# Optimization experiments

Hardware: AMD Instinct MI355X
Metric: run time of the kernel (lower is better)

## Reference

```python
import jax, jax.numpy as jnp
import numpy as np

EPS_LN = 1e-5
NEG_SLOPE = 0.2
NUM_GRAPHS = 64


def layer_norm(h, g, b):
    mu = h.mean(-1, keepdims=True)
    var = ((h - mu) ** 2).mean(-1, keepdims=True)
    return (h - mu) * jax.lax.rsqrt(var + EPS_LN) * g + b


def segment_softmax(alpha, dst, n):
    # alpha: [E2, H], softmax over edges sharing the same dst node
    m = jax.ops.segment_max(alpha, dst, num_segments=n)
    m = jnp.where(jnp.isfinite(m), m, 0.0)
    e = jnp.exp(alpha - m[dst])
    s = jax.ops.segment_sum(e, dst, num_segments=n)
    return e / (s[dst] + 1e-16)


def gat_conv(h, src, dst, eattr, W, We, a_s, a_d, a_e, bias, H, C):
    # PyG GATConv: shared src/dst linear, edge features, self-loops (fill='mean')
    N = h.shape[0]
    x = (h @ W).reshape(N, H, C)  # [N,H,C]
    loop = jnp.arange(N)
    src2 = jnp.concatenate([src, loop])
    dst2 = jnp.concatenate([dst, loop])
    loop_attr = jnp.broadcast_to(eattr.mean(0, keepdims=True), (N, eattr.shape[1]))
    e2 = jnp.concatenate([eattr, loop_attr], 0)
    eh = (e2 @ We).reshape(-1, H, C)  # [E2,H,C]
    alpha = (x * a_s).sum(-1)[src2] + (x * a_d).sum(-1)[dst2] + (eh * a_e).sum(-1)
    alpha = jax.nn.leaky_relu(alpha, NEG_SLOPE)  # [E2,H]
    alpha = segment_softmax(alpha, dst2, N)
    out = jax.ops.segment_sum(x[src2] * alpha[:, :, None], dst2, num_segments=N)
    return out.reshape(N, H * C) + bias


def setup_inputs():
    key = jax.random.key(0)
    ks = jax.random.split(key, 24)
    N, E = 50000, 400000
    Fin, Hd, H, ed = 6, 64, 4, 1
    d0 = Hd * H          # 256 after layer0
    C1 = 128 // H        # 32, layer1 per-head out
    s = 0.1
    inp = {
        'x': jax.random.normal(ks[0], (N, Fin), jnp.float32),
        'edge_index': jax.random.randint(ks[1], (2, E), 0, N),
        'edge_attr': jax.random.uniform(ks[2], (E, ed), jnp.float32),
        'batch': jnp.sort(jax.random.randint(ks[3], (N,), 0, NUM_GRAPHS)),
        'W_in': jax.random.normal(ks[4], (Fin, Hd), jnp.float32) * s,
        'b_in': jnp.zeros((Hd,), jnp.float32),
        'l0_W': jax.random.normal(ks[5], (Hd, H * Hd), jnp.float32) * s,
        'l0_We': jax.random.normal(ks[6], (ed, H * Hd), jnp.float32) * s,
        'l0_as': jax.random.normal(ks[7], (H, Hd), jnp.float32) * s,
        'l0_ad': jax.random.normal(ks[8], (H, Hd), jnp.float32) * s,
        'l0_ae': jax.random.normal(ks[9], (H, Hd), jnp.float32) * s,
        'l0_b': jnp.zeros((H * Hd,), jnp.float32),
        'ln0_g': jnp.ones((d0,), jnp.float32),
        'ln0_b': jnp.zeros((d0,), jnp.float32),
        'l1_W': jax.random.normal(ks[10], (d0, H * C1), jnp.float32) * s,
        'l1_We': jax.random.normal(ks[11], (ed, H * C1), jnp.float32) * s,
        'l1_as': jax.random.normal(ks[12], (H, C1), jnp.float32) * s,
        'l1_ad': jax.random.normal(ks[13], (H, C1), jnp.float32) * s,
        'l1_ae': jax.random.normal(ks[14], (H, C1), jnp.float32) * s,
        'l1_b': jnp.zeros((H * C1,), jnp.float32),
        'ln1_g': jnp.ones((128,), jnp.float32),
        'ln1_b': jnp.zeros((128,), jnp.float32),
    }
    return inp


def reference(x, edge_index, edge_attr, batch, W_in, b_in,
              l0_W, l0_We, l0_as, l0_ad, l0_ae, l0_b, ln0_g, ln0_b,
              l1_W, l1_We, l1_as, l1_ad, l1_ae, l1_b, ln1_g, ln1_b):
    src, dst = edge_index[0], edge_index[1]
    H = 4
    h = x @ W_in + b_in                                  # input_proj
    h = gat_conv(h, src, dst, edge_attr, l0_W, l0_We, l0_as, l0_ad, l0_ae, l0_b, H, 64)
    h = layer_norm(h, ln0_g, ln0_b)
    h = jax.nn.elu(h)                                    # dropout off (eval)
    h = gat_conv(h, src, dst, edge_attr, l1_W, l1_We, l1_as, l1_ad, l1_ae, l1_b, H, 32)
    h = layer_norm(h, ln1_g, ln1_b)
    cnt = jax.ops.segment_sum(jnp.ones((h.shape[0],), h.dtype), batch, num_segments=NUM_GRAPHS)
    h_mean = jax.ops.segment_sum(h, batch, num_segments=NUM_GRAPHS) / jnp.maximum(cnt, 1.0)[:, None]
    h_max = jax.ops.segment_max(h, batch, num_segments=NUM_GRAPHS)
    return (h_mean + h_max) / 2.0
```

## Files before the change

kernel.cpp:

```cpp
#include <hip/hip_runtime.h>
#include <math.h>

#define EPS_LN   1e-5f
#define NEG_SLOPE 0.2f
#define NUM_GRAPHS 64
#define POOL_SPLIT 16

__device__ __forceinline__ float red64(float v) {
    #pragma unroll
    for (int m = 32; m > 0; m >>= 1) v += __shfl_xor(v, m);
    return v;
}

__global__ __launch_bounds__(256) void k_input_proj(
    const float* __restrict__ x, const float* __restrict__ Win,
    const float* __restrict__ bin, float* __restrict__ h, int N)
{
    int t = blockIdx.x * 256 + threadIdx.x;
    if (t >= N * 64) return;
    int n = t >> 6, c = t & 63;
    float acc = bin[c];
    const float* xr = x + n * 6;
    #pragma unroll
    for (int k = 0; k < 6; ++k) acc += xr[k] * Win[k * 64 + c];
    h[t] = acc;
}

__global__ __launch_bounds__(256) void k_prep(
    const float* __restrict__ We0, const float* __restrict__ ae0,
    const float* __restrict__ We1, const float* __restrict__ ae1,
    float* __restrict__ wedot0, float* __restrict__ wedot1)
{
    __shared__ float red[256];
    int t = threadIdx.x;
    red[t] = We0[t] * ae0[t];
    __syncthreads();
    for (int s = 32; s > 0; s >>= 1) { if ((t & 63) < s) red[t] += red[t + s]; __syncthreads(); }
    if ((t & 63) == 0) wedot0[t >> 6] = red[t];
    __syncthreads();
    red[t] = (t < 128) ? We1[t] * ae1[t] : 0.f;
    __syncthreads();
    for (int s = 16; s > 0; s >>= 1) { if (t < 128 && (t & 31) < s) red[t] += red[t + s]; __syncthreads(); }
    if (t < 128 && (t & 31) == 0) wedot1[t >> 5] = red[t];
}

__global__ __launch_bounds__(256) void k_esum_partial(const float* __restrict__ ea, float* __restrict__ part, int E)
{
    __shared__ float red[256];
    int t = threadIdx.x;
    float s = 0.f;
    for (int i = blockIdx.x * 256 + t; i < E; i += gridDim.x * 256) s += ea[i];
    red[t] = s; __syncthreads();
    for (int k = 128; k > 0; k >>= 1) { if (t < k) red[t] += red[t + k]; __syncthreads(); }
    if (t == 0) part[blockIdx.x] = red[0];
}
__global__ __launch_bounds__(256) void k_esum_final(const float* __restrict__ part, int B, float* __restrict__ mean_out, int E)
{
    __shared__ float red[256];
    int t = threadIdx.x;
    red[t] = (t < B) ? part[t] : 0.f; __syncthreads();
    for (int k = 128; k > 0; k >>= 1) { if (t < k) red[t] += red[t + k]; __syncthreads(); }
    if (t == 0) *mean_out = red[0] / (float)E;
}

__global__ __launch_bounds__(256) void k_counts_init(int* __restrict__ counts, int N)
{
    int t = blockIdx.x * 256 + threadIdx.x;
    if (t < N) counts[t] = 1;
}
__global__ __launch_bounds__(256) void k_count(const int* __restrict__ dst, int* __restrict__ counts, int E)
{
    int e = blockIdx.x * 256 + threadIdx.x;
    if (e < E) atomicAdd(&counts[dst[e]], 1);
}
__global__ __launch_bounds__(256) void k_scan_partial(const int* __restrict__ counts, int* __restrict__ bsum, int N)
{
    __shared__ int red[256];
    int b = blockIdx.x, t = threadIdx.x;
    int base = b * 1024 + t * 4;
    int s = 0;
    #pragma unroll
    for (int i = 0; i < 4; ++i) { int idx = base + i; if (idx < N) s += counts[idx]; }
    red[t] = s; __syncthreads();
    for (int k = 128; k > 0; k >>= 1) { if (t < k) red[t] += red[t + k]; __syncthreads(); }
    if (t == 0) bsum[b] = red[0];
}
__global__ __launch_bounds__(64) void k_scan_bsums(const int* __restrict__ bsum, int* __restrict__ bpre, int B)
{
    __shared__ int s[64];
    int t = threadIdx.x;
    int v = (t < B) ? bsum[t] : 0;
    s[t] = v; __syncthreads();
    for (int off = 1; off < 64; off <<= 1) {
        int u = (t >= off) ? s[t - off] : 0; __syncthreads();
        s[t] += u; __syncthreads();
    }
    if (t < B) bpre[t] = s[t] - v;
}
__global__ __launch_bounds__(256) void k_scan_chunk(
    const int* __restrict__ counts, const int* __restrict__ bpre,
    int* __restrict__ row_ptr, int* __restrict__ cursor, int N, int E2)
{
    __shared__ int s[256];
    int b = blockIdx.x, t = threadIdx.x;
    int base = b * 1024 + t * 4;
    int l0 = (base + 0 < N) ? counts[base + 0] : 0;
    int l1 = (base + 1 < N) ? counts[base + 1] : 0;
    int l2 = (base + 2 < N) ? counts[base + 2] : 0;
    int l3 = (base + 3 < N) ? counts[base + 3] : 0;
    int lsum = l0 + l1 + l2 + l3;
    s[t] = lsum; __syncthreads();
    for (int off = 1; off < 256; off <<= 1) {
        int u = (t >= off) ? s[t - off] : 0; __syncthreads();
        s[t] += u; __syncthreads();
    }
    int run = bpre[b] + s[t] - lsum;
    if (base + 0 < N) { row_ptr[base + 0] = run; cursor[base + 0] = run; } run += l0;
    if (base + 1 < N) { row_ptr[base + 1] = run; cursor[base + 1] = run; } run += l1;
    if (base + 2 < N) { row_ptr[base + 2] = run; cursor[base + 2] = run; } run += l2;
    if (base + 3 < N) { row_ptr[base + 3] = run; cursor[base + 3] = run; }
    if (b == 0 && t == 0) row_ptr[N] = E2;
}
__global__ __launch_bounds__(256) void k_place(
    const int* __restrict__ dst, int* __restrict__ cursor, int* __restrict__ eids, int E, int N)
{
    int e = blockIdx.x * 256 + threadIdx.x;
    if (e >= E + N) return;
    int d = (e < E) ? dst[e] : (e - E);
    int pos = atomicAdd(&cursor[d], 1);
    eids[pos] = e;
}
__global__ __launch_bounds__(256) void k_rowsort(const int* __restrict__ row_ptr, int* __restrict__ eids, int N)
{
    int n = blockIdx.x * 256 + threadIdx.x;
    if (n >= N) return;
    int r0 = row_ptr[n], r1 = row_ptr[n + 1];
    for (int i = r0 + 1; i < r1; ++i) {
        int key = eids[i];
        int j = i - 1;
        while (j >= r0 && eids[j] > key) { eids[j + 1] = eids[j]; --j; }
        eids[j + 1] = key;
    }
}

#define G0_NPW 4
__global__ __launch_bounds__(256) void k_gemm0(
    const float* __restrict__ h, const float* __restrict__ W0,
    const float* __restrict__ As, const float* __restrict__ Ad,
    float* __restrict__ x0, float* __restrict__ as0, float* __restrict__ ad0, int N)
{
    __shared__ float Wl[64 * 256];
    int t = threadIdx.x;
    for (int i = t; i < 64 * 256; i += 256) Wl[i] = W0[i];
    __syncthreads();
    int wave = t >> 6, lane = t & 63;
    float asv[4], adv[4];
    #pragma unroll
    for (int j = 0; j < 4; ++j) { asv[j] = As[j * 64 + lane]; adv[j] = Ad[j * 64 + lane]; }
    int gw = blockIdx.x * 4 + wave;
    int stride = gridDim.x * 4 * G0_NPW;
    for (int nb = gw * G0_NPW; nb < N; nb += stride) {
        float hv[G0_NPW];
        float acc[G0_NPW][4] = {};
        #pragma unroll
        for (int p = 0; p < G0_NPW; ++p) {
            int n = nb + p;
            hv[p] = (n < N) ? h[(size_t)n * 64 + lane] : 0.f;
        }
        for (int k = 0; k < 64; ++k) {
            float w0 = Wl[k * 256 + lane];
            float w1 = Wl[k * 256 + lane + 64];
            float w2 = Wl[k * 256 + lane + 128];
            float w3 = Wl[k * 256 + lane + 192];
            #pragma unroll
            for (int p = 0; p < G0_NPW; ++p) {
                float hk = __shfl(hv[p], k);
                acc[p][0] += hk * w0; acc[p][1] += hk * w1;
                acc[p][2] += hk * w2; acc[p][3] += hk * w3;
            }
        }
        #pragma unroll
        for (int p = 0; p < G0_NPW; ++p) {
            int n = nb + p;
            if (n < N) {
                float* o = x0 + (size_t)n * 256;
                o[lane] = acc[p][0]; o[lane + 64] = acc[p][1];
                o[lane + 128] = acc[p][2]; o[lane + 192] = acc[p][3];
            }
            #pragma unroll
            for (int j = 0; j < 4; ++j) {
                float ps = red64(acc[p][j] * asv[j]);
                float pd = red64(acc[p][j] * adv[j]);
                if (lane == 0 && n < N) { as0[n * 4 + j] = ps; ad0[n * 4 + j] = pd; }
            }
        }
    }
}

__global__ __launch_bounds__(256) void k_gemm1(
    const float* __restrict__ h0, const float* __restrict__ W1,
    const float* __restrict__ As, const float* __restrict__ Ad,
    float* __restrict__ x1, float* __restrict__ as1, float* __restrict__ ad1, int N)
{
    __shared__ float Wc[32 * 128];
    __shared__ float Ht[32 * 128];
    const int nb = blockIdx.x * 128;
    const int t = threadIdx.x;
    const int tc = t & 15, tr = t >> 4;
    const int r0 = tr * 4, c0 = tc * 4;
    const int kg = t & 7, rb = t >> 3;
    float asv[8], adv[8];
    #pragma unroll
    for (int j = 0; j < 8; ++j) {
        int col = c0 + ((j < 4) ? j : 60 + j);
        asv[j] = As[col]; adv[j] = Ad[col];
    }
    float acc[8][8] = {};
    for (int kc = 0; kc < 8; ++kc) {
        __syncthreads();
        #pragma unroll
        for (int j = 0; j < 4; ++j) {
            int row = rb + j * 32;
            int n = nb + row;
            float4 v = make_float4(0.f, 0.f, 0.f, 0.f);
            if (n < N)
                v = *reinterpret_cast<const float4*>(h0 + (size_t)n * 256 + kc * 32 + kg * 4);
            #pragma unroll
            for (int i = 0; i < 4; ++i) {
                int k = kg * 4 + i;
                float e = (i == 0) ? v.x : (i == 1) ? v.y : (i == 2) ? v.z : v.w;
                Ht[k * 128 + (row ^ (k & 28))] = e;
            }
        }
        #pragma unroll
        for (int it = 0; it < 4; ++it) {
            int idx = t * 4 + it * 1024;
            int k2 = idx >> 7, c = idx & 127;
            *reinterpret_cast<float4*>(&Wc[idx]) =
                *reinterpret_cast<const float4*>(W1 + (size_t)(kc * 32 + k2) * 128 + c);
        }
        __syncthreads();
        #pragma unroll 4
        for (int k2 = 0; k2 < 32; ++k2) {
            int sw = k2 & 28;
            float4 hlo = *reinterpret_cast<const float4*>(&Ht[k2 * 128 + (r0 ^ sw)]);
            float4 hhi = *reinterpret_cast<const float4*>(&Ht[k2 * 128 + ((r0 + 64) ^ sw)]);
            float4 wlo = *reinterpret_cast<const float4*>(&Wc[k2 * 128 + c0]);
            float4 whi = *reinterpret_cast<const float4*>(&Wc[k2 * 128 + c0 + 64]);
            float hr[8] = {hlo.x, hlo.y, hlo.z, hlo.w, hhi.x, hhi.y, hhi.z, hhi.w};
            float wr[8] = {wlo.x, wlo.y, wlo.z, wlo.w, whi.x, whi.y, whi.z, whi.w};
            #pragma unroll
            for (int i = 0; i < 8; ++i)
                #pragma unroll
                for (int j = 0; j < 8; ++j)
                    acc[i][j] += hr[i] * wr[j];
        }
    }
    #pragma unroll
    for (int i = 0; i < 8; ++i) {
        int n = nb + ((i < 4) ? (r0 + i) : (r0 + 60 + i));
        if (n < N) {
            *reinterpret_cast<float4*>(x1 + (size_t)n * 128 + c0) =
                make_float4(acc[i][0], acc[i][1], acc[i][2], acc[i][3]);
            *reinterpret_cast<float4*>(x1 + (size_t)n * 128 + c0 + 64) =
                make_float4(acc[i][4], acc[i][5], acc[i][6], acc[i][7]);
        }
        float sA = acc[i][0] * asv[0] + acc[i][1] * asv[1] + acc[i][2] * asv[2] + acc[i][3] * asv[3];
        float sB = acc[i][4] * asv[4] + acc[i][5] * asv[5] + acc[i][6] * asv[6] + acc[i][7] * asv[7];
        float dA = acc[i][0] * adv[0] + acc[i][1] * adv[1] + acc[i][2] * adv[2] + acc[i][3] * adv[3];
        float dB = acc[i][4] * adv[4] + acc[i][5] * adv[5] + acc[i][6] * adv[6] + acc[i][7] * adv[7];
        #pragma unroll
        for (int off = 1; off <= 4; off <<= 1) {
            sA += __shfl_xor(sA, off); sB += __shfl_xor(sB, off);
            dA += __shfl_xor(dA, off); dB += __shfl_xor(dB, off);
        }
        if ((tc & 7) == 0 && n < N) {
            int hA = tc >> 3;
            as1[n * 4 + hA] = sA; as1[n * 4 + 2 + hA] = sB;
            ad1[n * 4 + hA] = dA; ad1[n * 4 + 2 + hA] = dB;
        }
    }
}

template <bool WRITE_SRC>
__global__ __launch_bounds__(256) void k_edgeprep(
    const int* __restrict__ row_ptr, const int* __restrict__ eids,
    const int* __restrict__ src, const float* __restrict__ eattr,
    const float* __restrict__ emean_p, const float* __restrict__ wedot,
    const float* __restrict__ as_n, const float* __restrict__ ad_n,
    int* __restrict__ srcp, float4* __restrict__ alpha, float* __restrict__ sinv,
    int N, int E)
{
    int n = (blockIdx.x * 256 + threadIdx.x) >> 6;
    int lane = threadIdx.x & 63;
    if (n >= N) return;
    float emean = *emean_p;
    float wd0 = wedot[0], wd1 = wedot[1], wd2 = wedot[2], wd3 = wedot[3];
    float adv0 = ad_n[n * 4 + 0], adv1 = ad_n[n * 4 + 1];
    float adv2 = ad_n[n * 4 + 2], adv3 = ad_n[n * 4 + 3];
    int r0 = row_ptr[n], r1 = row_ptr[n + 1];

    float m0 = -1e30f, m1 = -1e30f, m2 = -1e30f, m3 = -1e30f;
    for (int i = r0 + lane; i < r1; i += 64) {
        int eid = eids[i];
        int sn; float ev;
        if (eid < E) { sn = src[eid]; ev = eattr[eid]; } else { sn = n; ev = emean; }
        if (WRITE_SRC) srcp[i] = sn;
        const float* as4 = as_n + (size_t)sn * 4;
        float a0 = as4[0] + adv0 + ev * wd0;
        float a1 = as4[1] + adv1 + ev * wd1;
        float a2 = as4[2] + adv2 + ev * wd2;
        float a3 = as4[3] + adv3 + ev * wd3;
        a0 = (a0 > 0.f) ? a0 : NEG_SLOPE * a0;
        a1 = (a1 > 0.f) ? a1 : NEG_SLOPE * a1;
        a2 = (a2 > 0.f) ? a2 : NEG_SLOPE * a2;
        a3 = (a3 > 0.f) ? a3 : NEG_SLOPE * a3;
        m0 = fmaxf(m0, a0); m1 = fmaxf(m1, a1);
        m2 = fmaxf(m2, a2); m3 = fmaxf(m3, a3);
        alpha[i] = make_float4(a0, a1, a2, a3);
    }
    #pragma unroll
    for (int off = 32; off > 0; off >>= 1) {
        m0 = fmaxf(m0, __shfl_xor(m0, off));
        m1 = fmaxf(m1, __shfl_xor(m1, off));
        m2 = fmaxf(m2, __shfl_xor(m2, off));
        m3 = fmaxf(m3, __shfl_xor(m3, off));
    }
    float s0 = 0.f, s1 = 0.f, s2 = 0.f, s3 = 0.f;
    for (int i = r0 + lane; i < r1; i += 64) {
        float4 a = alpha[i];
        float w0 = __expf(a.x - m0), w1 = __expf(a.y - m1);
        float w2 = __expf(a.z - m2), w3 = __expf(a.w - m3);
        s0 += w0; s1 += w1; s2 += w2; s3 += w3;
        alpha[i] = make_float4(w0, w1, w2, w3);
    }
    #pragma unroll
    for (int off = 32; off > 0; off >>= 1) {
        s0 += __shfl_xor(s0, off); s1 += __shfl_xor(s1, off);
        s2 += __shfl_xor(s2, off); s3 += __shfl_xor(s3, off);
    }
    if (lane == 0) {
        sinv[n * 4 + 0] = 1.f / (s0 + 1e-16f);
        sinv[n * 4 + 1] = 1.f / (s1 + 1e-16f);
        sinv[n * 4 + 2] = 1.f / (s2 + 1e-16f);
        sinv[n * 4 + 3] = 1.f / (s3 + 1e-16f);
    }
}

template <int HC, int VEC, bool DO_ELU>
__global__ __launch_bounds__(256) void k_agg(
    const float* __restrict__ x, const int* __restrict__ row_ptr,
    const int* __restrict__ srcp, const float* __restrict__ alpha,
    const float* __restrict__ sinv,
    const float* __restrict__ bias, const float* __restrict__ lng, const float* __restrict__ lnb,
    float* __restrict__ out, int N)
{
    int n = (blockIdx.x * 256 + threadIdx.x) >> 6;
    int lane = threadIdx.x & 63;
    if (n >= N) return;
    int hh = lane >> 4;
    int r0 = row_ptr[n], r1 = row_ptr[n + 1];

    float acc[VEC] = {};
    for (int i = r0; i < r1; i += 8) {
        int cnt = min(r1 - i, 8);
        int sn[8]; float wv[8];
        #pragma unroll
        for (int j = 0; j < 8; ++j)
            if (j < cnt) { sn[j] = srcp[i + j]; wv[j] = alpha[(size_t)(i + j) * 4 + hh]; }
        #pragma unroll
        for (int j = 0; j < 8; ++j)
            if (j < cnt) {
                const float* xr = x + (size_t)sn[j] * HC + lane * VEC;
                if constexpr (VEC == 4) {
                    float4 xv = *reinterpret_cast<const float4*>(xr);
                    acc[0] += wv[j] * xv.x; acc[1] += wv[j] * xv.y;
                    acc[2] += wv[j] * xv.z; acc[3] += wv[j] * xv.w;
                } else {
                    float2 xv = *reinterpret_cast<const float2*>(xr);
                    acc[0] += wv[j] * xv.x; acc[1] += wv[j] * xv.y;
                }
            }
    }
    float inv = sinv[n * 4 + hh];

    int ch0 = lane * VEC;
    float v[VEC];
    #pragma unroll
    for (int i = 0; i < VEC; ++i) v[i] = acc[i] * inv + bias[ch0 + i];
    float ls = 0.f;
    #pragma unroll
    for (int i = 0; i < VEC; ++i) ls += v[i];
    ls = red64(ls);
    float mu = ls / (float)HC;
    float lv = 0.f;
    #pragma unroll
    for (int i = 0; i < VEC; ++i) { float d = v[i] - mu; lv += d * d; }
    lv = red64(lv);
    float rs = rsqrtf(lv / (float)HC + EPS_LN);
    float o[VEC];
    #pragma unroll
    for (int i = 0; i < VEC; ++i) {
        float y = (v[i] - mu) * rs * lng[ch0 + i] + lnb[ch0 + i];
        if (DO_ELU) y = (y > 0.f) ? y : (expm1f(y));
        o[i] = y;
    }
    float* orow = out + (size_t)n * HC + ch0;
    if constexpr (VEC == 4) *reinterpret_cast<float4*>(orow) = make_float4(o[0], o[1], o[2], o[3]);
    else                    *reinterpret_cast<float2*>(orow) = make_float2(o[0], o[1]);
}

__global__ __launch_bounds__(128) void k_bounds(const int* __restrict__ batch, int* __restrict__ gstart, int N)
{
    int g = threadIdx.x;
    if (g > NUM_GRAPHS) return;
    int lo = 0, hi = N;
    while (lo < hi) { int mid = (lo + hi) >> 1; if (batch[mid] < g) lo = mid + 1; else hi = mid; }
    gstart[g] = lo;
}
__global__ __launch_bounds__(128) void k_pool1(
    const float* __restrict__ h1, const int* __restrict__ gstart,
    float* __restrict__ psum, float* __restrict__ pmax)
{
    int g = blockIdx.x, sl = blockIdx.y, c = threadIdx.x;
    int s0 = gstart[g], s1 = gstart[g + 1];
    int cnt = s1 - s0;
    int chunk = (cnt + POOL_SPLIT - 1) / POOL_SPLIT;
    int b0 = s0 + sl * chunk;
    int b1 = min(b0 + chunk, s1);
    float sum = 0.f, mx = -INFINITY;
    for (int n = b0; n < b1; ++n) {
        float v = h1[(size_t)n * 128 + c];
        sum += v; mx = fmaxf(mx, v);
    }
    int o = (g * POOL_SPLIT + sl) * 128 + c;
    psum[o] = sum; pmax[o] = mx;
}
__global__ __launch_bounds__(128) void k_pool2(
    const float* __restrict__ psum, const float* __restrict__ pmax,
    const int* __restrict__ gstart, float* __restrict__ out)
{
    int g = blockIdx.x, c = threadIdx.x;
    float sum = 0.f, mx = -INFINITY;
    #pragma unroll
    for (int sl = 0; sl < POOL_SPLIT; ++sl) {
        int o = (g * POOL_SPLIT + sl) * 128 + c;
        sum += psum[o];
        mx = fmaxf(mx, pmax[o]);
    }
    int cnt = gstart[g + 1] - gstart[g];
    float mean = sum / fmaxf((float)cnt, 1.f);
    out[g * 128 + c] = 0.5f * (mean + mx);
}

extern "C" void kernel_launch(void* const* d_in, const int* in_sizes, int n_in,
                              void* d_out, int out_size, void* d_ws, size_t ws_size,
                              hipStream_t stream)
{
    const float* x     = (const float*)d_in[0];
    const int*   ei    = (const int*)d_in[1];
    const float* eattr = (const float*)d_in[2];
    const int*   batch = (const int*)d_in[3];
    const float* Win   = (const float*)d_in[4];
    const float* bin   = (const float*)d_in[5];
    const float* l0W   = (const float*)d_in[6];
    const float* l0We  = (const float*)d_in[7];
    const float* l0as  = (const float*)d_in[8];
    const float* l0ad  = (const float*)d_in[9];
    const float* l0ae  = (const float*)d_in[10];
    const float* l0b   = (const float*)d_in[11];
    const float* ln0g  = (const float*)d_in[12];
    const float* ln0b  = (const float*)d_in[13];
    const float* l1W   = (const float*)d_in[14];
    const float* l1We  = (const float*)d_in[15];
    const float* l1as  = (const float*)d_in[16];
    const float* l1ad  = (const float*)d_in[17];
    const float* l1ae  = (const float*)d_in[18];
    const float* l1b   = (const float*)d_in[19];
    const float* ln1g  = (const float*)d_in[20];
    const float* ln1b  = (const float*)d_in[21];

    const int N = in_sizes[0] / 6;
    const int E = in_sizes[1] / 2;
    const int E2 = E + N;
    const int* srcI = ei;
    const int* dstI = ei + E;

    char* ws = (char*)d_ws;
    size_t off = 0;
    auto alloc = [&](size_t bytes) -> char* {
        char* p = ws + off;
        off += (bytes + 255) & ~(size_t)255;
        return p;
    };

    float* h      = (float*)alloc((size_t)N * 64 * 4);
    float* x0     = (float*)alloc((size_t)N * 256 * 4);
    float* h0     = (float*)alloc((size_t)N * 256 * 4);
    float* as0    = (float*)alloc((size_t)N * 4 * 4);
    float* ad0    = (float*)alloc((size_t)N * 4 * 4);
    float* as1    = (float*)alloc((size_t)N * 4 * 4);
    float* ad1    = (float*)alloc((size_t)N * 4 * 4);
    float* sinv   = (float*)alloc((size_t)N * 4 * 4);
    int*   row_ptr= (int*)alloc((size_t)(N + 1) * 4);
    int*   counts = (int*)alloc((size_t)N * 4);
    int*   cursor = (int*)alloc((size_t)N * 4);
    int*   eids   = (int*)alloc((size_t)E2 * 4);
    int*   srcp   = (int*)alloc((size_t)E2 * 4);
    float4* alphab= (float4*)alloc((size_t)E2 * 16);
    int*   bsum   = (int*)alloc(64 * 4);
    int*   bpre   = (int*)alloc(64 * 4);
    float* epart  = (float*)alloc(256 * 4);
    float* emean  = (float*)alloc(4);
    float* wedot0 = (float*)alloc(16);
    float* wedot1 = (float*)alloc(16);
    int*   gstart = (int*)alloc((NUM_GRAPHS + 1) * 4);
    float* psum   = (float*)alloc((size_t)NUM_GRAPHS * POOL_SPLIT * 128 * 4);
    float* pmax   = (float*)alloc((size_t)NUM_GRAPHS * POOL_SPLIT * 128 * 4);

    float* x1 = x0;
    float* h1 = x0 + (size_t)N * 128;

    const int B = (N + 1023) / 1024;

    k_input_proj<<<(N * 64 + 255) / 256, 256, 0, stream>>>(x, Win, bin, h, N);
    k_prep<<<1, 256, 0, stream>>>(l0We, l0ae, l1We, l1ae, wedot0, wedot1);
    k_esum_partial<<<256, 256, 0, stream>>>(eattr, epart, E);
    k_esum_final<<<1, 256, 0, stream>>>(epart, 256, emean, E);

    k_counts_init<<<(N + 255) / 256, 256, 0, stream>>>(counts, N);
    k_count<<<(E + 255) / 256, 256, 0, stream>>>(dstI, counts, E);
    k_scan_partial<<<B, 256, 0, stream>>>(counts, bsum, N);
    k_scan_bsums<<<1, 64, 0, stream>>>(bsum, bpre, B);
    k_scan_chunk<<<B, 256, 0, stream>>>(counts, bpre, row_ptr, cursor, N, E2);
    k_place<<<(E2 + 255) / 256, 256, 0, stream>>>(dstI, cursor, eids, E, N);
    k_rowsort<<<(N + 255) / 256, 256, 0, stream>>>(row_ptr, eids, N);

    k_gemm0<<<512, 256, 0, stream>>>(h, l0W, l0as, l0ad, x0, as0, ad0, N);
    k_edgeprep<true><<<(N + 3) / 4, 256, 0, stream>>>(
        row_ptr, eids, srcI, eattr, emean, wedot0, as0, ad0, srcp, alphab, sinv, N, E);
    k_agg<256, 4, true><<<(N + 3) / 4, 256, 0, stream>>>(
        x0, row_ptr, srcp, (const float*)alphab, sinv, l0b, ln0g, ln0b, h0, N);

    k_gemm1<<<(N + 127) / 128, 256, 0, stream>>>(h0, l1W, l1as, l1ad, x1, as1, ad1, N);
    k_edgeprep<false><<<(N + 3) / 4, 256, 0, stream>>>(
        row_ptr, eids, srcI, eattr, emean, wedot1, as1, ad1, srcp, alphab, sinv, N, E);
    k_agg<128, 2, false><<<(N + 3) / 4, 256, 0, stream>>>(
        x1, row_ptr, srcp, (const float*)alphab, sinv, l1b, ln1g, ln1b, h1, N);

    k_bounds<<<1, 128, 0, stream>>>(batch, gstart, N);
    k_pool1<<<dim3(NUM_GRAPHS, POOL_SPLIT), 128, 0, stream>>>(h1, gstart, psum, pmax);
    k_pool2<<<NUM_GRAPHS, 128, 0, stream>>>(psum, pmax, gstart, (float*)d_out);
}
```

Measured before the change: 442.8 us.

## Rewrite layer-0 GEMM as shared-memory tiled 8x8 register-blocked kernel

Replaces the wave-per-node-group GEMM that broadcast h via shuffles against a full 64x256 weight table in LDS with a 128-node by 128-column tiled kernel. It is launched on a 2D grid over node tiles and column halves, stages transposed, XOR-swizzled h tiles and weight chunks in LDS, and accumulates an 8x8 register tile per thread. Attention source/destination dot products are reduced with 16-lane shuffles per head. The aim is to raise arithmetic intensity and cut shuffle and LDS traffic per FMA, at the cost of more registers and a larger grid.

Result: faster. 391.7 us (-11.6%).

```diff
diff --git a/kernel.cpp b/kernel.cpp
--- a/kernel.cpp
+++ b/kernel.cpp
@@ -143,56 +143,88 @@
     }
 }
 
-#define G0_NPW 4
 __global__ __launch_bounds__(256) void k_gemm0(
     const float* __restrict__ h, const float* __restrict__ W0,
     const float* __restrict__ As, const float* __restrict__ Ad,
     float* __restrict__ x0, float* __restrict__ as0, float* __restrict__ ad0, int N)
 {
-    __shared__ float Wl[64 * 256];
-    int t = threadIdx.x;
-    for (int i = t; i < 64 * 256; i += 256) Wl[i] = W0[i];
-    __syncthreads();
-    int wave = t >> 6, lane = t & 63;
-    float asv[4], adv[4];
-    #pragma unroll
-    for (int j = 0; j < 4; ++j) { asv[j] = As[j * 64 + lane]; adv[j] = Ad[j * 64 + lane]; }
-    int gw = blockIdx.x * 4 + wave;
-    int stride = gridDim.x * 4 * G0_NPW;
-    for (int nb = gw * G0_NPW; nb < N; nb += stride) {
-        float hv[G0_NPW];
-        float acc[G0_NPW][4] = {};
-        #pragma unroll
-        for (int p = 0; p < G0_NPW; ++p) {
-            int n = nb + p;
-            hv[p] = (n < N) ? h[(size_t)n * 64 + lane] : 0.f;
-        }
-        for (int k = 0; k < 64; ++k) {
-            float w0 = Wl[k * 256 + lane];
-            float w1 = Wl[k * 256 + lane + 64];
-            float w2 = Wl[k * 256 + lane + 128];
-            float w3 = Wl[k * 256 + lane + 192];
+    __shared__ float Wc[32 * 128];
+    __shared__ float Ht[32 * 128];
+    const int nb = blockIdx.x * 128;
+    const int q  = blockIdx.y;
+    const int t = threadIdx.x;
+    const int tc = t & 15, tr = t >> 4;
+    const int r0 = tr * 4, c0 = tc * 4;
+    const int kg = t & 7, rb = t >> 3;
+    float asv[8], adv[8];
+    #pragma unroll
+    for (int j = 0; j < 8; ++j) {
+        int col = q * 128 + c0 + ((j < 4) ? j : 60 + j);
+        asv[j] = As[col]; adv[j] = Ad[col];
+    }
+    float acc[8][8] = {};
+    #pragma unroll
+    for (int kc = 0; kc < 2; ++kc) {
+        __syncthreads();
+        #pragma unroll
+        for (int j = 0; j < 4; ++j) {
+            int row = rb + j * 32;
+            int n = nb + row;
+            float4 v = make_float4(0.f, 0.f, 0.f, 0.f);
+            if (n < N)
+                v = *reinterpret_cast<const float4*>(h + (size_t)n * 64 + kc * 32 + kg * 4);
             #pragma unroll
-            for (int p = 0; p < G0_NPW; ++p) {
-                float hk = __shfl(hv[p], k);
-                acc[p][0] += hk * w0; acc[p][1] += hk * w1;
-                acc[p][2] += hk * w2; acc[p][3] += hk * w3;
+            for (int i = 0; i < 4; ++i) {
+                int k = kg * 4 + i;
+                float e = (i == 0) ? v.x : (i == 1) ? v.y : (i == 2) ? v.z : v.w;
+                Ht[k * 128 + (row ^ (k & 28))] = e;
             }
         }
         #pragma unroll
-        for (int p = 0; p < G0_NPW; ++p) {
-            int n = nb + p;
-            if (n < N) {
-                float* o = x0 + (size_t)n * 256;
-                o[lane] = acc[p][0]; o[lane + 64] = acc[p][1];
-                o[lane + 128] = acc[p][2]; o[lane + 192] = acc[p][3];
-            }
+        for (int it = 0; it < 4; ++it) {
+            int idx = t * 4 + it * 1024;
+            int k2 = idx >> 7, c = idx & 127;
+            *reinterpret_cast<float4*>(&Wc[idx]) =
+                *reinterpret_cast<const float4*>(W0 + (size_t)(kc * 32 + k2) * 256 + q * 128 + c);
+        }
+        __syncthreads();
+        #pragma unroll 4
+        for (int k2 = 0; k2 < 32; ++k2) {
+            int sw = k2 & 28;
+            float4 hlo = *reinterpret_cast<const float4*>(&Ht[k2 * 128 + (r0 ^ sw)]);
+            float4 hhi = *reinterpret_cast<const float4*>(&Ht[k2 * 128 + ((r0 + 64) ^ sw)]);
+            float4 wlo = *reinterpret_cast<const float4*>(&Wc[k2 * 128 + c0]);
+            float4 whi = *reinterpret_cast<const float4*>(&Wc[k2 * 128 + c0 + 64]);
+            float hr[8] = {hlo.x, hlo.y, hlo.z, hlo.w, hhi.x, hhi.y, hhi.z, hhi.w};
+            float wr[8] = {wlo.x, wlo.y, wlo.z, wlo.w, whi.x, whi.y, whi.z, whi.w};
             #pragma unroll
-            for (int j = 0; j < 4; ++j) {
-                float ps = red64(acc[p][j] * asv[j]);
-                float pd = red64(acc[p][j] * adv[j]);
-                if (lane == 0 && n < N) { as0[n * 4 + j] = ps; ad0[n * 4 + j] = pd; }
-            }
+            for (int i = 0; i < 8; ++i)
+                #pragma unroll
+                for (int j = 0; j < 8; ++j)
+                    acc[i][j] += hr[i] * wr[j];
+        }
+    }
+    #pragma unroll
+    for (int i = 0; i < 8; ++i) {
+        int n = nb + ((i < 4) ? (r0 + i) : (r0 + 60 + i));
+        if (n < N) {
+            *reinterpret_cast<float4*>(x0 + (size_t)n * 256 + q * 128 + c0) =
+                make_float4(acc[i][0], acc[i][1], acc[i][2], acc[i][3]);
+            *reinterpret_cast<float4*>(x0 + (size_t)n * 256 + q * 128 + c0 + 64) =
+                make_float4(acc[i][4], acc[i][5], acc[i][6], acc[i][7]);
+        }
+        float sA = acc[i][0] * asv[0] + acc[i][1] * asv[1] + acc[i][2] * asv[2] + acc[i][3] * asv[3];
+        float sB = acc[i][4] * asv[4] + acc[i][5] * asv[5] + acc[i][6] * asv[6] + acc[i][7] * asv[7];
+        float dA = acc[i][0] * adv[0] + acc[i][1] * adv[1] + acc[i][2] * adv[2] + acc[i][3] * adv[3];
+        float dB = acc[i][4] * adv[4] + acc[i][5] * adv[5] + acc[i][6] * adv[6] + acc[i][7] * adv[7];
+        #pragma unroll
+        for (int off = 1; off <= 8; off <<= 1) {
+            sA += __shfl_xor(sA, off); sB += __shfl_xor(sB, off);
+            dA += __shfl_xor(dA, off); dB += __shfl_xor(dB, off);
+        }
+        if (tc == 0 && n < N) {
+            as0[n * 4 + 2 * q] = sA; as0[n * 4 + 2 * q + 1] = sB;
+            ad0[n * 4 + 2 * q] = dA; ad0[n * 4 + 2 * q + 1] = dB;
         }
     }
 }
@@ -536,7 +568,7 @@
     k_place<<<(E2 + 255) / 256, 256, 0, stream>>>(dstI, cursor, eids, E, N);
     k_rowsort<<<(N + 255) / 256, 256, 0, stream>>>(row_ptr, eids, N);
 
-    k_gemm0<<<512, 256, 0, stream>>>(h, l0W, l0as, l0ad, x0, as0, ad0, N);
+    k_gemm0<<<dim3((N + 127) / 128, 2), 256, 0, stream>>>(h, l0W, l0as, l0ad, x0, as0, ad0, N);
     k_edgeprep<true><<<(N + 3) / 4, 256, 0, stream>>>(
         row_ptr, eids, srcI, eattr, emean, wedot0, as0, ad0, srcp, alphab, sinv, N, E);
     k_agg<256, 4, true><<<(N + 3) / 4, 256, 0, stream>>>(
```
